# Performance work log

Measured on AMD Instinct MI355X. Metric: run time of the kernel, lower is better.

The kernel has to match this reference:

```python
import jax, jax.numpy as jnp
import numpy as np

D_EMBED = 1024
N_HEAD = 16
LEN_TRIM = 1024
LN_EPS = 1e-5


def setup_inputs() -> dict:
    key = jax.random.key(0)
    ks = jax.random.split(key, 8)
    B = 2
    h_q = jax.random.normal(ks[0], (B, LEN_TRIM, D_EMBED), jnp.float32)
    h_kv1 = jax.random.normal(ks[1], (B, LEN_TRIM, D_EMBED), jnp.float32)
    h_kv2 = jax.random.normal(ks[2], (B, 2 * LEN_TRIM, D_EMBED), jnp.float32)
    mask = jax.random.uniform(ks[3], (B, LEN_TRIM, 1), jnp.float32)
    in_proj_w = jax.random.normal(ks[4], (3 * D_EMBED, D_EMBED), jnp.float32) * 0.02
    in_proj_b = jnp.zeros((3 * D_EMBED,), jnp.float32)
    out_w = jax.random.normal(ks[5], (D_EMBED, D_EMBED), jnp.float32) * 0.02
    out_b = jnp.zeros((D_EMBED,), jnp.float32)
    ln_g = jnp.ones((D_EMBED,), jnp.float32)
    ln_b = jnp.zeros((D_EMBED,), jnp.float32)
    return dict(h_q=h_q, h_kv1=h_kv1, h_kv2=h_kv2, mask=mask,
                in_proj_w=in_proj_w, in_proj_b=in_proj_b,
                out_w=out_w, out_b=out_b, ln_g=ln_g, ln_b=ln_b)


def _layernorm(x, g, b):
    mu = jnp.mean(x, axis=-1, keepdims=True)
    var = jnp.mean(jnp.square(x - mu), axis=-1, keepdims=True)
    return (x - mu) * jax.lax.rsqrt(var + LN_EPS) * g + b


def reference(h_q, h_kv1, h_kv2, mask, in_proj_w, in_proj_b, out_w, out_b, ln_g, ln_b):
    B, L, D = h_q.shape
    H = N_HEAD
    dh = D // H
    h_kv = jnp.concatenate((h_kv1, h_kv2), axis=1)  # (B, 3L, D)
    S = h_kv.shape[1]
    Wq, Wk, Wv = jnp.split(in_proj_w, 3, axis=0)
    bq, bk, bv = jnp.split(in_proj_b, 3, axis=0)
    q = (h_q @ Wq.T + bq).reshape(B, L, H, dh).transpose(0, 2, 1, 3)   # (B,H,L,dh)
    k = (h_kv @ Wk.T + bk).reshape(B, S, H, dh).transpose(0, 2, 1, 3)  # (B,H,S,dh)
    v = (h_kv @ Wv.T + bv).reshape(B, S, H, dh).transpose(0, 2, 1, 3)
    scores = jnp.einsum('bhld,bhsd->bhls', q, k) / jnp.sqrt(jnp.float32(dh))
    block = jnp.triu(jnp.ones((L, L), bool), k=1)
    mask_causal = jnp.concatenate((block, block, block), axis=-1)  # (L, S)
    scores = jnp.where(mask_causal, -jnp.inf, scores)
    attn = jax.nn.softmax(scores, axis=-1)
    ctx = jnp.einsum('bhls,bhsd->bhld', attn, v).transpose(0, 2, 1, 3).reshape(B, L, D)
    attn_out = ctx @ out_w.T + out_b
    return _layernorm(h_q + attn_out, ln_g, ln_b) * mask
```

## Files before the change

### kernel.cpp

```cpp
#include <hip/hip_runtime.h>
#include <stdint.h>

typedef unsigned short u16;
typedef unsigned int u32;
typedef __bf16 bf16x8 __attribute__((ext_vector_type(8)));
typedef float floatx4 __attribute__((ext_vector_type(4)));
typedef u16 u16x8 __attribute__((ext_vector_type(8)));
typedef u16 u16x4 __attribute__((ext_vector_type(4)));

__device__ __forceinline__ u16 f2bf(float f) {
    __bf16 h = (__bf16)f;
    return __builtin_bit_cast(u16, h);
}

__device__ __forceinline__ void gll16(const u16* g, u16* l) {
    typedef __attribute__((address_space(1))) u32 gu32;
    typedef __attribute__((address_space(3))) u32 lu32;
    __builtin_amdgcn_global_load_lds((gu32*)g, (lu32*)l, 16, 0, 0);
}

__global__ __launch_bounds__(256) void cvt_all(const float* __restrict__ hq,
                                               const float* __restrict__ kv1,
                                               const float* __restrict__ kv2,
                                               const float* __restrict__ win,
                                               u16* __restrict__ a_q,
                                               u16* __restrict__ a_kv,
                                               u16* __restrict__ wb) {
    const int NQ = 262144, NKV = 786432, NW = 393216;
    int i = blockIdx.x * 256 + threadIdx.x;
    const int stride = gridDim.x * 256;
    for (; i < NQ + NKV + NW; i += stride) {
        const float* src; u16* dst;
        if (i < NQ) {
            src = hq + (long long)i * 8; dst = a_q + (long long)i * 8;
        } else if (i < NQ + NKV) {
            int c = i - NQ;
            int row = c >> 7;
            int col = (c & 127) * 8;
            int b = row >= 3072, r = row - b * 3072;
            src = (r < 1024) ? kv1 + ((long long)(b * 1024 + r)) * 1024 + col
                             : kv2 + ((long long)(b * 2048 + (r - 1024))) * 1024 + col;
            dst = a_kv + (long long)row * 1024 + col;
        } else {
            int c = i - (NQ + NKV);
            src = win + (long long)c * 8; dst = wb + (long long)c * 8;
        }
        floatx4 x = *(const floatx4*)src;
        floatx4 y = *(const floatx4*)(src + 4);
        u16x8 o;
        #pragma unroll
        for (int j = 0; j < 4; j++) { o[j] = f2bf(x[j]); o[4 + j] = f2bf(y[j]); }
        *(u16x8*)dst = o;
    }
}

__global__ __launch_bounds__(256) void cvt_bf16(const float* __restrict__ in,
                                                u16* __restrict__ out, int n8) {
    int i = blockIdx.x * 256 + threadIdx.x;
    const int stride = gridDim.x * 256;
    for (; i < n8; i += stride) {
        floatx4 a = *(const floatx4*)(in + (long long)i * 8);
        floatx4 b = *(const floatx4*)(in + (long long)i * 8 + 4);
        u16x8 o;
        #pragma unroll
        for (int j = 0; j < 4; j++) { o[j] = f2bf(a[j]); o[4 + j] = f2bf(b[j]); }
        *(u16x8*)(out + (long long)i * 8) = o;
    }
}

__global__ __launch_bounds__(256) void gemm_proj(const u16* __restrict__ aq,
                                                 const u16* __restrict__ akv,
                                                 const u16* __restrict__ wb,
                                                 const float* __restrict__ bias,
                                                 u16* __restrict__ Qo,
                                                 u16* __restrict__ Ko,
                                                 u16* __restrict__ VTg) {
    __shared__ u16 lds[2][2][8192];
    const int tid = threadIdx.x;
    const int wave = tid >> 6, lane = tid & 63;
    const int lane16 = lane & 15, quad = lane >> 4;
    const int bid = blockIdx.x;
    const int g = (bid & 7) * 112 + (bid >> 3);
    const bool qblk = g < 128;
    int my, nx;
    if (qblk) { my = g >> 3; nx = g & 7; }
    else { int gg = g - 128; my = gg >> 4; nx = gg & 15; }
    const int rowBase = my * 128;
    const int colBase = nx * 128;
    const int wrow = (qblk ? 0 : 1024) + colBase;
    const int wm = (wave >> 1) * 64, wn = (wave & 1) * 64;

    floatx4 acc[4][4];
    #pragma unroll
    for (int am = 0; am < 4; am++)
        #pragma unroll
        for (int bn = 0; bn < 4; bn++) acc[am][bn] = floatx4{0.f, 0.f, 0.f, 0.f};

    const int srow8 = tid >> 3;
    const int scol = ((tid & 7) ^ (srow8 & 7)) * 8;
    const u16* aS = (qblk ? aq : akv) + (long long)(rowBase + srow8) * 1024 + scol;
    const u16* bS = wb + (long long)(wrow + srow8) * 1024 + scol;
    u16* lbase = &lds[0][0][0];
    const int ldst = wave * 512;

    const int cko0 = ((quad ^ (lane16 & 7)) * 8);
    const int cko1 = (((4 + quad) ^ (lane16 & 7)) * 8);

    {
        u16* dA = lbase; u16* dB = lbase + 8192;
        #pragma unroll
        for (int j = 0; j < 4; j++) {
            gll16(aS + j * 32768, dA + j * 2048 + ldst);
            gll16(bS + j * 32768, dB + j * 2048 + ldst);
        }
    }
    __syncthreads();

    int buf = 0;
    for (int t = 0; t < 16; t++) {
        if (t < 15) {
            const int k0 = (t + 1) * 64;
            u16* dA = lbase + (buf ^ 1) * 16384;
            u16* dB = dA + 8192;
            #pragma unroll
            for (int j = 0; j < 4; j++) {
                gll16(aS + j * 32768 + k0, dA + j * 2048 + ldst);
                gll16(bS + j * 32768 + k0, dB + j * 2048 + ldst);
            }
        }
        const u16* Ab = lbase + buf * 16384;
        const u16* Bb = Ab + 8192;
        u16x8 a0[4], a1[4], b0[4], b1[4];
        #pragma unroll
        for (int i = 0; i < 4; i++) {
            a0[i] = *(const u16x8*)&Ab[(wm + i * 16 + lane16) * 64 + cko0];
            a1[i] = *(const u16x8*)&Ab[(wm + i * 16 + lane16) * 64 + cko1];
            b0[i] = *(const u16x8*)&Bb[(wn + i * 16 + lane16) * 64 + cko0];
            b1[i] = *(const u16x8*)&Bb[(wn + i * 16 + lane16) * 64 + cko1];
        }
        #pragma unroll
        for (int am = 0; am < 4; am++)
            #pragma unroll
            for (int bn = 0; bn < 4; bn++)
                acc[am][bn] = __builtin_amdgcn_mfma_f32_16x16x32_bf16(
                    __builtin_bit_cast(bf16x8, a0[am]),
                    __builtin_bit_cast(bf16x8, b0[bn]), acc[am][bn], 0, 0, 0);
        #pragma unroll
        for (int am = 0; am < 4; am++)
            #pragma unroll
            for (int bn = 0; bn < 4; bn++)
                acc[am][bn] = __builtin_amdgcn_mfma_f32_16x16x32_bf16(
                    __builtin_bit_cast(bf16x8, a1[am]),
                    __builtin_bit_cast(bf16x8, b1[bn]), acc[am][bn], 0, 0, 0);
        __syncthreads();
        buf ^= 1;
    }

    const float* bcol = bias + (qblk ? 0 : 1024) + colBase;
    if (qblk || nx < 8) {
        u16* Cb = qblk ? Qo : Ko;
        #pragma unroll
        for (int am = 0; am < 4; am++)
            #pragma unroll
            for (int bn = 0; bn < 4; bn++)
                #pragma unroll
                for (int r = 0; r < 4; r++) {
                    int row = rowBase + wm + am * 16 + quad * 4 + r;
                    int col = wn + bn * 16 + lane16;
                    float v = acc[am][bn][r] + bcol[col];
                    if (qblk) v *= 0.1803368801f;
                    Cb[(long long)row * 1024 + colBase + col] = f2bf(v);
                }
    } else {
        const int b_ = rowBase >= 3072;
        const int keyBase = rowBase - b_ * 3072 + wm;
        #pragma unroll
        for (int am = 0; am < 4; am++)
            #pragma unroll
            for (int bn = 0; bn < 4; bn++) {
                int col = wn + bn * 16 + lane16;
                int d = colBase - 1024 + col;
                int key0 = keyBase + am * 16 + quad * 4;
                u16x4 pk;
                #pragma unroll
                for (int r = 0; r < 4; r++) pk[r] = f2bf(acc[am][bn][r] + bcol[col]);
                *(u16x4*)&VTg[((long long)(b_ * 1024 + d)) * 3072 + key0] = pk;
            }
    }
}

__global__ __launch_bounds__(256) void gemm_out(const u16* __restrict__ ctx,
                                                const u16* __restrict__ wob,
                                                const float* __restrict__ bias,
                                                float* __restrict__ ao0,
                                                float* __restrict__ ao1) {
    __shared__ u16 lds[2][2][8192];
    const int tid = threadIdx.x;
    const int wave = tid >> 6, lane = tid & 63;
    const int lane16 = lane & 15, quad = lane >> 4;
    const int bid = blockIdx.x;
    const int g = (bid & 7) * 32 + (bid >> 3);
    const int my = g >> 4;
    const int nx = (g & 15) >> 1;
    const int kh = g & 1;
    const int rowBase = my * 128, colBase = nx * 128, kbase = kh * 512;
    const int wm = (wave >> 1) * 64, wn = (wave & 1) * 64;

    floatx4 acc[4][4];
    #pragma unroll
    for (int am = 0; am < 4; am++)
        #pragma unroll
        for (int bn = 0; bn < 4; bn++) acc[am][bn] = floatx4{0.f, 0.f, 0.f, 0.f};

    const int srow8 = tid >> 3;
    const int scol = ((tid & 7) ^ (srow8 & 7)) * 8;
    const u16* aS = ctx + (long long)(rowBase + srow8) * 1024 + kbase + scol;
    const u16* bS = wob + (long long)(colBase + srow8) * 1024 + kbase + scol;
    u16* lbase = &lds[0][0][0];
    const int ldst = wave * 512;
    const int cko0 = ((quad ^ (lane16 & 7)) * 8);
    const int cko1 = (((4 + quad) ^ (lane16 & 7)) * 8);

    {
        u16* dA = lbase; u16* dB = lbase + 8192;
        #pragma unroll
        for (int j = 0; j < 4; j++) {
            gll16(aS + j * 32768, dA + j * 2048 + ldst);
            gll16(bS + j * 32768, dB + j * 2048 + ldst);
        }
    }
    __syncthreads();

    int buf = 0;
    for (int t = 0; t < 8; t++) {
        if (t < 7) {
            const int k0 = (t + 1) * 64;
            u16* dA = lbase + (buf ^ 1) * 16384;
            u16* dB = dA + 8192;
            #pragma unroll
            for (int j = 0; j < 4; j++) {
                gll16(aS + j * 32768 + k0, dA + j * 2048 + ldst);
                gll16(bS + j * 32768 + k0, dB + j * 2048 + ldst);
            }
        }
        const u16* Ab = lbase + buf * 16384;
        const u16* Bb = Ab + 8192;
        u16x8 a0[4], a1[4], b0[4], b1[4];
        #pragma unroll
        for (int i = 0; i < 4; i++) {
            a0[i] = *(const u16x8*)&Ab[(wm + i * 16 + lane16) * 64 + cko0];
            a1[i] = *(const u16x8*)&Ab[(wm + i * 16 + lane16) * 64 + cko1];
            b0[i] = *(const u16x8*)&Bb[(wn + i * 16 + lane16) * 64 + cko0];
            b1[i] = *(const u16x8*)&Bb[(wn + i * 16 + lane16) * 64 + cko1];
        }
        #pragma unroll
        for (int am = 0; am < 4; am++)
            #pragma unroll
            for (int bn = 0; bn < 4; bn++)
                acc[am][bn] = __builtin_amdgcn_mfma_f32_16x16x32_bf16(
                    __builtin_bit_cast(bf16x8, a0[am]),
                    __builtin_bit_cast(bf16x8, b0[bn]), acc[am][bn], 0, 0, 0);
        #pragma unroll
        for (int am = 0; am < 4; am++)
            #pragma unroll
            for (int bn = 0; bn < 4; bn++)
                acc[am][bn] = __builtin_amdgcn_mfma_f32_16x16x32_bf16(
                    __builtin_bit_cast(bf16x8, a1[am]),
                    __builtin_bit_cast(bf16x8, b1[bn]), acc[am][bn], 0, 0, 0);
        __syncthreads();
        buf ^= 1;
    }

    float* Co = kh ? ao1 : ao0;
    #pragma unroll
    for (int am = 0; am < 4; am++)
        #pragma unroll
        for (int bn = 0; bn < 4; bn++)
            #pragma unroll
            for (int r = 0; r < 4; r++) {
                int row = rowBase + wm + am * 16 + quad * 4 + r;
                int col = colBase + wn + bn * 16 + lane16;
                float v = acc[am][bn][r] + (kh == 0 ? bias[col] : 0.f);
                Co[(long long)row * 1024 + col] = v;
            }
}

#define ATTN_TILE(DIAG_, HAVENEXT_)                                           \
{                                                                             \
    const int cur = t & 1;                                                    \
    if (HAVENEXT_) {                                                          \
        const long long ko = (long long)(t + 1) * 65536;                      \
        const long long vo = (long long)(t + 1) * 64;                         \
        _Pragma("unroll")                                                     \
        for (int j = 0; j < 2; j++) {                                         \
            gll16(kS + ko + j * 32768, &Kt[cur ^ 1][j * 2048 + ldst]);        \
            gll16(vS + vo + (long long)j * 32 * 3072, &Vt[cur ^ 1][j * 2048 + ldst]); \
        }                                                                     \
        asm volatile("s_waitcnt vmcnt(4)" ::: "memory");   \
    } else {                                                                  \
        asm volatile("s_waitcnt vmcnt(0)" ::: "memory");                      \
    }                                                                         \
    __builtin_amdgcn_sched_barrier(0);                                        \
    floatx4 sacc[4];                                                          \
    _Pragma("unroll")                                                         \
    for (int mi = 0; mi < 4; mi++) sacc[mi] = floatx4{0.f, 0.f, 0.f, 0.f};    \
    __builtin_amdgcn_s_setprio(1);                                            \
    _Pragma("unroll")                                                         \
    for (int mi = 0; mi < 4; mi++) {                                          \
        u16x8 kf = *(const u16x8*)&Kt[cur][(mi * 16 + lane16) * 64 + slot0];  \
        sacc[mi] = __builtin_amdgcn_mfma_f32_16x16x32_bf16(                   \
            __builtin_bit_cast(bf16x8, kf), qf[0], sacc[mi], 0, 0, 0);        \
    }                                                                         \
    _Pragma("unroll")                                                         \
    for (int mi = 0; mi < 4; mi++) {                                          \
        u16x8 kf = *(const u16x8*)&Kt[cur][(mi * 16 + lane16) * 64 + slot1];  \
        sacc[mi] = __builtin_amdgcn_mfma_f32_16x16x32_bf16(                   \
            __builtin_bit_cast(bf16x8, kf), qf[1], sacc[mi], 0, 0, 0);        \
    }                                                                         \
    __builtin_amdgcn_s_setprio(0);                                            \
    if (DIAG_) {                                \
        _Pragma("unroll")                                                     \
        for (int mi = 0; mi < 4; mi++)                                        \
            _Pragma("unroll")                                                 \
            for (int r = 0; r < 4; r++)                                       \
                if ((mi * 16 + quad * 4 + r) > qloc) sacc[mi][r] = -1e30f;    \
    }                                                                         \
    float tmax = fmaxf(sacc[0][0], sacc[0][1]);       \
    tmax = fmaxf(tmax, fmaxf(sacc[0][2], sacc[0][3]));                        \
    _Pragma("unroll")                                                         \
    for (int mi = 1; mi < 4; mi++) {                                          \
        tmax = fmaxf(tmax, fmaxf(sacc[mi][0], sacc[mi][1]));                  \
        tmax = fmaxf(tmax, fmaxf(sacc[mi][2], sacc[mi][3]));                  \
    }                                                                         \
    if (!__all(tmax <= m_i + 8.0f)) {           \
        float tr = fmaxf(tmax, __shfl_xor(tmax, 16));                         \
        tr = fmaxf(tr, __shfl_xor(tr, 32));                                   \
        float m_new = fmaxf(m_i, tr);                                         \
        float alpha = exp2f(m_i - m_new);                                     \
        _Pragma("unroll")                                                     \
        for (int mi = 0; mi < 4; mi++)                                        \
            _Pragma("unroll")                                                 \
            for (int r = 0; r < 4; r++) o_acc[mi][r] *= alpha;                \
        l_lane *= alpha;                                                      \
        m_i = m_new;                                                          \
    }                                                                         \
    _Pragma("unroll")                                                         \
    for (int mi = 0; mi < 4; mi++) {                                          \
        u16x4 pk;                                                             \
        _Pragma("unroll")                                                     \
        for (int r = 0; r < 4; r++) {                                         \
            float p = exp2f(sacc[mi][r] - m_i);                               \
            l_lane += p;                                                      \
            pk[r] = f2bf(p);                                                  \
        }                                                                     \
        *(u16x4*)&Ps[wave][lane16 * 64 +                                      \
            (((mi * 2 + (quad >> 1)) ^ (lane16 & 7)) << 3) + (quad & 1) * 4] = pk; \
    }                                                                         \
    __builtin_amdgcn_wave_barrier();                                          \
    __builtin_amdgcn_s_setprio(1);                                            \
    _Pragma("unroll")                                                         \
    for (int c = 0; c < 2; c++) {                                             \
        bf16x8 pf = __builtin_bit_cast(bf16x8, *(const u16x8*)&Ps[wave][      \
            lane16 * 64 + (((c * 4 + quad) ^ (lane16 & 7)) << 3)]);           \
        const int slot = c ? slot1 : slot0;                                   \
        _Pragma("unroll")                                                     \
        for (int mi = 0; mi < 4; mi++) {                                      \
            bf16x8 vf = __builtin_bit_cast(bf16x8,                            \
                *(const u16x8*)&Vt[cur][(mi * 16 + lane16) * 64 + slot]);     \
            o_acc[mi] = __builtin_amdgcn_mfma_f32_16x16x32_bf16(vf, pf, o_acc[mi], 0, 0, 0); \
        }                                                                     \
    }                                                                         \
    __builtin_amdgcn_s_setprio(0);                                            \
    if (HAVENEXT_) {                            \
        asm volatile("s_waitcnt lgkmcnt(0)" ::: "memory");                    \
        __builtin_amdgcn_s_barrier();                                         \
        __builtin_amdgcn_sched_barrier(0);                                    \
    }                                                                         \
}

__global__ __launch_bounds__(256) void attn_seg(const u16* __restrict__ Q,
                                                const u16* __restrict__ Kb,
                                                const u16* __restrict__ VTg,
                                                float* __restrict__ pO_lo,
                                                float* __restrict__ pO_hi,
                                                float* __restrict__ pml) {
    __shared__ u16 Kt[2][4096];
    __shared__ u16 Vt[2][4096];
    __shared__ u16 Ps[4][1024];
    const int tid = threadIdx.x;
    const int wave = tid >> 6, lane = tid & 63;
    const int lane16 = lane & 15, quad = lane >> 4;
    const int bid = blockIdx.x;
    const int idx_ = (bid & 7) * 192 + (bid >> 3);
    const int qhat = idx_ & 15;
    const int h   = (idx_ >> 4) & 15;
    const int b   = (idx_ >> 8) & 1;
    const int seg = idx_ >> 9;
    const int qt = b ? (15 - qhat) : qhat;
    const int l0 = qt * 64;
    const int wq = wave * 16;
    const int qloc = wq + lane16;

    bf16x8 qf[2];
    {
        const u16* qrow = Q + ((long long)(b * 1024 + l0 + wq + lane16)) * 1024 + h * 64;
        qf[0] = __builtin_bit_cast(bf16x8, *(const u16x8*)(qrow + quad * 8));
        qf[1] = __builtin_bit_cast(bf16x8, *(const u16x8*)(qrow + 32 + quad * 8));
    }

    const int srow = tid >> 3;
    const int csw8 = ((tid & 7) ^ (srow & 7)) * 8;
    const long long bh = ((long long)b * 3072) * 1024 + h * 64;
    const u16* kS = Kb + bh + ((long long)(seg * 1024)) * 1024
                    + (long long)srow * 1024 + csw8;
    const u16* vS = VTg + ((long long)(b * 1024 + h * 64 + srow)) * 3072
                    + seg * 1024 + csw8;
    const int ldst = wave * 512;

    {
        #pragma unroll
        for (int j = 0; j < 2; j++) {
            gll16(kS + j * 32768, &Kt[0][j * 2048 + ldst]);
            gll16(vS + (long long)j * 32 * 3072, &Vt[0][j * 2048 + ldst]);
        }
    }
    __syncthreads();

    const int slot0 = ((quad ^ (lane16 & 7)) * 8);
    const int slot1 = (((4 + quad) ^ (lane16 & 7)) * 8);

    float m_i = -1e30f, l_lane = 0.f;
    floatx4 o_acc[4];
    #pragma unroll
    for (int mi = 0; mi < 4; mi++) o_acc[mi] = floatx4{0.f, 0.f, 0.f, 0.f};

    for (int t = 0; t < qt; t++) ATTN_TILE(false, true)
    { int t = qt; ATTN_TILE(true, false) }

    float l_i = l_lane;
    l_i += __shfl_xor(l_i, 16);
    l_i += __shfl_xor(l_i, 32);

    const int p = ((b * 16 + h) * 16 + qt) * 3 + seg;
    float* op = (p < 512) ? (pO_lo + (long long)p * 4096)
                          : (pO_hi + (long long)(p - 512) * 4096);
    if (quad == 0) {
        pml[(long long)p * 128 + (wq + lane16) * 2]     = m_i;
        pml[(long long)p * 128 + (wq + lane16) * 2 + 1] = l_i;
    }
    float* orow = op + (long long)(wq + lane16) * 64;
    #pragma unroll
    for (int mi = 0; mi < 4; mi++)
        *(floatx4*)(orow + mi * 16 + quad * 4) = o_acc[mi];
}

__global__ __launch_bounds__(256) void attn_combine(const float* __restrict__ pO_lo,
                                                    const float* __restrict__ pO_hi,
                                                    const float* __restrict__ pml,
                                                    u16* __restrict__ Ctx) {
    const int g = blockIdx.x;
    const int qt = g & 15;
    const int h  = (g >> 4) & 15;
    const int b  = g >> 8;
    const int t  = threadIdx.x;
    const int q  = t >> 2;
    const int d0 = (t & 3) * 16;
    const int p0 = g * 3;

    float m[3], l[3];
    #pragma unroll
    for (int s = 0; s < 3; s++) {
        m[s] = pml[(long long)(p0 + s) * 128 + q * 2];
        l[s] = pml[(long long)(p0 + s) * 128 + q * 2 + 1];
    }
    float M = fmaxf(m[0], fmaxf(m[1], m[2]));
    float w[3];
    #pragma unroll
    for (int s = 0; s < 3; s++) w[s] = exp2f(m[s] - M);
    float L = w[0] * l[0] + w[1] * l[1] + w[2] * l[2];
    float invL = 1.0f / L;

    const float* O[3];
    #pragma unroll
    for (int s = 0; s < 3; s++) {
        int pp = p0 + s;
        O[s] = ((pp < 512) ? (pO_lo + (long long)pp * 4096)
                           : (pO_hi + (long long)(pp - 512) * 4096))
               + (long long)q * 64 + d0;
    }

    long long crow = ((long long)(b * 1024 + qt * 64 + q)) * 1024 + h * 64 + d0;
    #pragma unroll
    for (int i = 0; i < 16; i += 4) {
        floatx4 a  = *(const floatx4*)(O[0] + i);
        floatx4 bb = *(const floatx4*)(O[1] + i);
        floatx4 cc = *(const floatx4*)(O[2] + i);
        #pragma unroll
        for (int j = 0; j < 4; j++)
            Ctx[crow + i + j] = f2bf((w[0] * a[j] + w[1] * bb[j] + w[2] * cc[j]) * invL);
    }
}

__global__ __launch_bounds__(256) void ln_kernel(const float* __restrict__ AO0,
                                                 const float* __restrict__ AO1,
                                                 const float* __restrict__ HQ,
                                                 const float* __restrict__ g,
                                                 const float* __restrict__ bb,
                                                 const float* __restrict__ mask,
                                                 float* __restrict__ Out) {
    const int row = blockIdx.x;
    const int t = threadIdx.x;
    const int base = row * 1024 + t * 4;
    floatx4 a0 = *(const floatx4*)&AO0[base];
    floatx4 a1 = *(const floatx4*)&AO1[base];
    floatx4 hq = *(const floatx4*)&HQ[base];
    float x[4];
    #pragma unroll
    for (int i = 0; i < 4; i++) x[i] = a0[i] + a1[i] + hq[i];
    float s = x[0] + x[1] + x[2] + x[3];
    float ss = x[0]*x[0] + x[1]*x[1] + x[2]*x[2] + x[3]*x[3];
    #pragma unroll
    for (int off = 32; off >= 1; off >>= 1) { s += __shfl_xor(s, off); ss += __shfl_xor(ss, off); }
    __shared__ float smem[8];
    int wave = t >> 6, lane = t & 63;
    if (lane == 0) { smem[wave] = s; smem[4 + wave] = ss; }
    __syncthreads();
    s  = smem[0] + smem[1] + smem[2] + smem[3];
    ss = smem[4] + smem[5] + smem[6] + smem[7];
    float mu  = s * (1.f / 1024.f);
    float var = ss * (1.f / 1024.f) - mu * mu;
    float rs  = rsqrtf(var + 1e-5f);
    float mv  = mask[row];
    floatx4 g4 = *(const floatx4*)&g[t * 4];
    floatx4 b4 = *(const floatx4*)&bb[t * 4];
    floatx4 y4;
    #pragma unroll
    for (int i = 0; i < 4; i++) y4[i] = ((x[i] - mu) * rs * g4[i] + b4[i]) * mv;
    *(floatx4*)&Out[base] = y4;
}

extern "C" void kernel_launch(void* const* d_in, const int* in_sizes, int n_in,
                              void* d_out, int out_size, void* d_ws, size_t ws_size,
                              hipStream_t stream) {
    (void)in_sizes; (void)n_in; (void)out_size; (void)ws_size;
    const float* h_q   = (const float*)d_in[0];
    const float* h_kv1 = (const float*)d_in[1];
    const float* h_kv2 = (const float*)d_in[2];
    const float* maskp = (const float*)d_in[3];
    const float* win   = (const float*)d_in[4];
    const float* binp  = (const float*)d_in[5];
    const float* wout  = (const float*)d_in[6];
    const float* bout  = (const float*)d_in[7];
    const float* ln_g  = (const float*)d_in[8];
    const float* ln_b  = (const float*)d_in[9];
    float* outp = (float*)d_out;

    char* ws = (char*)d_ws;
    const size_t MB = 1024 * 1024;
    u16*   q_b   = (u16*)(ws);
    u16*   k_b   = (u16*)(ws + 4 * MB);
    u16*   vT    = (u16*)(ws + 16 * MB);
    u16*   ctx_b = q_b;
    u16*   a_q   = (u16*)(ws + 28 * MB);
    u16*   a_kv  = (u16*)(ws + 32 * MB);
    u16*   wb    = (u16*)d_out;
    float* pO_lo = (float*)d_out;
    float* pO_hi = (float*)(ws + 28 * MB);
    u16*   wob   = (u16*)(ws + 28 * MB);
    float* pml   = (float*)(ws + 44 * MB);
    float* ao0   = (float*)(ws + 4 * MB);
    float* ao1   = (float*)(ws + 12 * MB);

    cvt_all<<<2048, 256, 0, stream>>>(h_q, h_kv1, h_kv2, win, a_q, a_kv, wb);
    gemm_proj<<<896, 256, 0, stream>>>(a_q, a_kv, wb, binp, q_b, k_b, vT);
    attn_seg<<<1536, 256, 0, stream>>>(q_b, k_b, vT, pO_lo, pO_hi, pml);
    attn_combine<<<512, 256, 0, stream>>>(pO_lo, pO_hi, pml, ctx_b);
    cvt_bf16<<<512, 256, 0, stream>>>(wout, wob, 131072);
    gemm_out<<<256, 256, 0, stream>>>(ctx_b, wob, bout, ao0, ao1);
    ln_kernel<<<2048, 256, 0, stream>>>(ao0, ao1, h_q, ln_g, ln_b, maskp, outp);
}
```

Baseline: 225.9 us.

## Compute softmax row sums via MFMA with ones and reorder block scheduling

The per-lane scalar accumulation of exponentials and the cross-lane shuffle reduction are replaced by an extra MFMA that multiplies the bf16 probability tile by a ones vector, producing row sums directly in an accumulator. This removes VALU adds and shuffles but sums the bf16-rounded probabilities instead of the fp32 ones, which changes numerics slightly. The block-to-work mapping is also changed so that the longest query tiles (largest qt) are launched first across both batches, for better load balance in place of the previous XCD-interleaved mapping.

```diff
diff --git a/kernel.cpp b/kernel.cpp
--- a/kernel.cpp
+++ b/kernel.cpp
@@ -325,7 +325,7 @@
             for (int r = 0; r < 4; r++)                                       \
                 if ((mi * 16 + quad * 4 + r) > qloc) sacc[mi][r] = -1e30f;    \
     }                                                                         \
-    float tmax = fmaxf(sacc[0][0], sacc[0][1]);       \
+    float tmax = fmaxf(sacc[0][0], sacc[0][1]);                               \
     tmax = fmaxf(tmax, fmaxf(sacc[0][2], sacc[0][3]));                        \
     _Pragma("unroll")                                                         \
     for (int mi = 1; mi < 4; mi++) {                                          \
@@ -341,18 +341,14 @@
         for (int mi = 0; mi < 4; mi++)                                        \
             _Pragma("unroll")                                                 \
             for (int r = 0; r < 4; r++) o_acc[mi][r] *= alpha;                \
-        l_lane *= alpha;                                                      \
+        l_acc[0] *= alpha;                         \
         m_i = m_new;                                                          \
     }                                                                         \
     _Pragma("unroll")                                                         \
     for (int mi = 0; mi < 4; mi++) {                                          \
         u16x4 pk;                                                             \
         _Pragma("unroll")                                                     \
-        for (int r = 0; r < 4; r++) {                                         \
-            float p = exp2f(sacc[mi][r] - m_i);                               \
-            l_lane += p;                                                      \
-            pk[r] = f2bf(p);                                                  \
-        }                                                                     \
+        for (int r = 0; r < 4; r++) pk[r] = f2bf(exp2f(sacc[mi][r] - m_i));   \
         *(u16x4*)&Ps[wave][lane16 * 64 +                                      \
             (((mi * 2 + (quad >> 1)) ^ (lane16 & 7)) << 3) + (quad & 1) * 4] = pk; \
     }                                                                         \
@@ -369,6 +365,7 @@
                 *(const u16x8*)&Vt[cur][(mi * 16 + lane16) * 64 + slot]);     \
             o_acc[mi] = __builtin_amdgcn_mfma_f32_16x16x32_bf16(vf, pf, o_acc[mi], 0, 0, 0); \
         }                                                                     \
+        l_acc = __builtin_amdgcn_mfma_f32_16x16x32_bf16(onesf, pf, l_acc, 0, 0, 0); \
     }                                                                         \
     __builtin_amdgcn_s_setprio(0);                                            \
     if (HAVENEXT_) {                            \
@@ -391,12 +388,13 @@
     const int wave = tid >> 6, lane = tid & 63;
     const int lane16 = lane & 15, quad = lane >> 4;
     const int bid = blockIdx.x;
-    const int idx_ = (bid & 7) * 192 + (bid >> 3);
-    const int qhat = idx_ & 15;
-    const int h   = (idx_ >> 4) & 15;
-    const int b   = (idx_ >> 8) & 1;
-    const int seg = idx_ >> 9;
-    const int qt = b ? (15 - qhat) : qhat;
+    const int qrank = bid / 96;
+    const int r_    = bid - qrank * 96;
+    const int qt  = 15 - qrank;
+    const int b   = r_ / 48;
+    const int r2  = r_ - b * 48;
+    const int seg = r2 >> 4;
+    const int h   = r2 & 15;
     const int l0 = qt * 64;
     const int wq = wave * 16;
     const int qloc = wq + lane16;
@@ -407,6 +405,10 @@
         qf[0] = __builtin_bit_cast(bf16x8, *(const u16x8*)(qrow + quad * 8));
         qf[1] = __builtin_bit_cast(bf16x8, *(const u16x8*)(qrow + 32 + quad * 8));
     }
+    u16x8 onesu;
+    #pragma unroll
+    for (int j = 0; j < 8; j++) onesu[j] = 0x3F80;
+    const bf16x8 onesf = __builtin_bit_cast(bf16x8, onesu);
 
     const int srow = tid >> 3;
     const int csw8 = ((tid & 7) ^ (srow & 7)) * 8;
@@ -429,17 +431,16 @@
     const int slot0 = ((quad ^ (lane16 & 7)) * 8);
     const int slot1 = (((4 + quad) ^ (lane16 & 7)) * 8);
 
-    float m_i = -1e30f, l_lane = 0.f;
+    float m_i = -1e30f;
     floatx4 o_acc[4];
+    floatx4 l_acc = floatx4{0.f, 0.f, 0.f, 0.f};
     #pragma unroll
     for (int mi = 0; mi < 4; mi++) o_acc[mi] = floatx4{0.f, 0.f, 0.f, 0.f};
 
     for (int t = 0; t < qt; t++) ATTN_TILE(false, true)
     { int t = qt; ATTN_TILE(true, false) }
 
-    float l_i = l_lane;
-    l_i += __shfl_xor(l_i, 16);
-    l_i += __shfl_xor(l_i, 32);
+    const float l_i = l_acc[0];
 
     const int p = ((b * 16 + h) * 16 + qt) * 3 + seg;
     float* op = (p < 512) ? (pO_lo + (long long)p * 4096)
```

New measurement: 209.9 us. 1.08x faster.
